# Kernel tuning notes

Hardware: AMD Instinct MI355X
Metric: run time of the kernel (lower is better)

The kernel has to match this reference:

```python
import jax, jax.numpy as jnp
import numpy as np

MAX_DEPTH = 9
HIDDEN = 64
EMB = 64
POS_FREQS = 6
IN_C = 1
SIZES = [4 ** d for d in range(MAX_DEPTH + 1)]
OFFSETS = np.concatenate([[0], np.cumsum(SIZES)])  # per-depth slices into concatenated node arrays
TOTAL = int(OFFSETS[-1])  # 349525
POS_DIM = 3 + 2 * POS_FREQS * 3  # 39


def _interleave(v):
    v = v & 0xFFFF
    v = (v | (v << 8)) & 0x00FF00FF
    v = (v | (v << 4)) & 0x0F0F0F0F
    v = (v | (v << 2)) & 0x33333333
    v = (v | (v << 1)) & 0x55555555
    return v


def _deinterleave(v):
    v = v & 0x55555555
    v = (v | (v >> 1)) & 0x33333333
    v = (v | (v >> 2)) & 0x0F0F0F0F
    v = (v | (v >> 4)) & 0x00FF00FF
    v = (v | (v >> 8)) & 0x0000FFFF
    return v


def _xy(d):
    keys = jnp.arange(4 ** d, dtype=jnp.int32)  # full tree: sorted Morton keys = arange
    return _deinterleave(keys), _deinterleave(keys >> 1)


def _neighbors(d):
    # [N, 9] neighbor indices in Morton order grid; -1 outside the image (matches quadtree.neighs padding)
    ix, iy = _xy(d)
    res = 1 << d
    cols = []
    for dy in (-1, 0, 1):
        for dx in (-1, 0, 1):
            nx, ny = ix + dx, iy + dy
            valid = (nx >= 0) & (nx < res) & (ny >= 0) & (ny < res)
            key = _interleave(nx) | (_interleave(ny) << 1)
            cols.append(jnp.where(valid, key, -1))
    return jnp.stack(cols, axis=1)


def _pos_enc(d):
    # node_centers_from_keys + fourier_encode
    ix, iy = _xy(d)
    res = float(1 << d)
    x = (ix.astype(jnp.float32) + 0.5) / res
    y = (iy.astype(jnp.float32) + 0.5) / res
    dn = jnp.full_like(x, float(d) / float(MAX_DEPTH))
    pos = jnp.stack([x, y, dn], axis=1)  # [N, 3]
    freqs = 2.0 ** jnp.arange(POS_FREQS, dtype=jnp.float32)
    ang = pos[:, :, None] * (2.0 * np.pi) * freqs  # [N, 3, F]
    enc = jnp.concatenate([jnp.sin(ang), jnp.cos(ang)], axis=-1).reshape(pos.shape[0], -1)  # [N, 3*2F]
    return jnp.concatenate([pos, enc], axis=1)  # [N, 39]


def setup_inputs() -> dict:
    key = jax.random.key(0)
    ks = jax.random.split(key, 10)
    s = 0.05
    return {
        "features_in": jax.random.normal(ks[0], (TOTAL, IN_C), jnp.float32),
        "in_proj_W": jax.random.normal(ks[1], (IN_C + POS_DIM, HIDDEN), jnp.float32) * s,
        "in_proj_b": jnp.zeros((HIDDEN,), jnp.float32),
        "conv_W": jax.random.normal(ks[2], (MAX_DEPTH + 1, 9 * HIDDEN, HIDDEN), jnp.float32) * s,
        "conv_b": jnp.zeros((MAX_DEPTH + 1, HIDDEN), jnp.float32),
        "emb_W": jax.random.normal(ks[3], (MAX_DEPTH + 1, HIDDEN, EMB), jnp.float32) * s,
        "emb_b": jnp.zeros((MAX_DEPTH + 1, EMB), jnp.float32),
        "ln_g": jnp.ones((MAX_DEPTH + 1, EMB), jnp.float32),
        "ln_b": jnp.zeros((MAX_DEPTH + 1, EMB), jnp.float32),
        "depth_gain": jnp.ones((MAX_DEPTH + 1,), jnp.float32),
    }


def reference(features_in, in_proj_W, in_proj_b, conv_W, conv_b, emb_W, emb_b, ln_g, ln_b, depth_gain):
    D = MAX_DEPTH
    # per-depth input projection with fourier positional encoding
    h = []
    for d in range(D + 1):
        f = features_in[OFFSETS[d]:OFFSETS[d + 1]]
        x = jnp.concatenate([f, _pos_enc(d)], axis=1)  # [N_d, in_c + 39]
        h.append(x @ in_proj_W + in_proj_b)
    # bottom-up: QuadPool (mean over 4 children; full tree => children of parent i are 4i..4i+3) + QuadConv
    for d in range(D, 0, -1):
        Np = 4 ** (d - 1)
        pooled = h[d].reshape(Np, 4, HIDDEN).mean(axis=1)
        hd1 = h[d - 1] + pooled
        if d - 1 >= 1:
            neigh = _neighbors(d - 1)  # [N, 9], -1 at borders
            N = neigh.shape[0]
            padded = jnp.concatenate([hd1, jnp.zeros((1, HIDDEN), hd1.dtype)], axis=0)
            gi = jnp.where(neigh < 0, N, neigh)
            col = padded[gi].reshape(N, 9 * HIDDEN)
            hd1 = jax.nn.relu(col @ conv_W[d - 1] + conv_b[d - 1])
        h[d - 1] = hd1
    # per-depth embedding head: Linear -> LayerNorm -> depth gain
    outs = []
    eps = 1e-5
    for d in range(D + 1):
        z = h[d] @ emb_W[d] + emb_b[d]
        mu = z.mean(-1, keepdims=True)
        var = ((z - mu) ** 2).mean(-1, keepdims=True)
        z = (z - mu) / jnp.sqrt(var + eps) * ln_g[d] + ln_b[d]
        outs.append(depth_gain[d] * z)
    return jnp.concatenate(outs, axis=0)  # [TOTAL, EMB] (E[0]..E[max_depth] concatenated)
```

## Files before the change

### kernel.cpp

```cpp
#include <hip/hip_runtime.h>
#include <hip/hip_bf16.h>

static constexpr int TOTAL = 349525;
static constexpr int OFFS[11] = {0,1,5,21,85,341,1365,5461,21845,87381,349525};
static constexpr int EB64[11] = {0,1,2,3,4,8,24,88,344,1368,5464};
static constexpr size_t CONV_USH = (size_t)8*9*2*4*64*8;
static constexpr size_t EMB_USH  = (size_t)10*2*4*64*8;
static constexpr size_t FRAG_USH = CONV_USH + EMB_USH;
static constexpr size_t FRAG_BYTES = FRAG_USH*2*2;
static constexpr size_t HPRE_BYTES = (size_t)(87381-85)*64*4;

typedef __attribute__((ext_vector_type(8))) short short8;
typedef __attribute__((ext_vector_type(4))) float f32x4;

__device__ __forceinline__ unsigned deint(unsigned v){
  v &= 0x55555555u;
  v = (v | (v>>1)) & 0x33333333u;
  v = (v | (v>>2)) & 0x0F0F0F0Fu;
  v = (v | (v>>4)) & 0x00FF00FFu;
  v = (v | (v>>8)) & 0x0000FFFFu;
  return v;
}
__device__ __forceinline__ unsigned ileave(unsigned v){
  v &= 0xFFFFu;
  v = (v | (v<<8)) & 0x00FF00FFu;
  v = (v | (v<<4)) & 0x0F0F0F0Fu;
  v = (v | (v<<2)) & 0x33333333u;
  v = (v | (v<<1)) & 0x55555555u;
  return v;
}
__device__ __forceinline__ unsigned short f2bh(float x){
  unsigned u = __float_as_uint(x);
  return (unsigned short)((u + 0x7FFFu + ((u>>16)&1u)) >> 16);
}
__device__ __forceinline__ float bh2f(unsigned short h){
  return __uint_as_float(((unsigned)h) << 16);
}
__device__ __forceinline__ void split8(float4 a, float4 b, short8 &hi, short8 &lo){
  float v[8] = {a.x,a.y,a.z,a.w,b.x,b.y,b.z,b.w};
  unsigned short hv[8], lv[8];
  #pragma unroll
  for (int j=0;j<8;++j){ hv[j]=f2bh(v[j]); lv[j]=f2bh(v[j]-bh2f(hv[j])); }
  hi = short8{(short)hv[0],(short)hv[1],(short)hv[2],(short)hv[3],
              (short)hv[4],(short)hv[5],(short)hv[6],(short)hv[7]};
  lo = short8{(short)lv[0],(short)lv[1],(short)lv[2],(short)lv[3],
              (short)lv[4],(short)lv[5],(short)lv[6],(short)lv[7]};
}

__global__ __launch_bounds__(256) void k_wprep(const float* __restrict__ convW,
    const float* __restrict__ embW,
    unsigned short* __restrict__ WH, unsigned short* __restrict__ WLo){
  int tid = blockIdx.x*256 + threadIdx.x;
  if (tid >= 41984) return;
  const float* src;
  size_t dst;
  if (tid < 36864){
    int l=tid&63, cb=(tid>>6)&3, ks=(tid>>8)&1;
    int x=tid>>9; int m=x%9, Lp=x/9;
    int k0=ks*32+((l>>4)<<3), ch=cb*16+(l&15);
    src = convW + (size_t)(Lp+1)*36864 + (size_t)(m*64+k0)*64 + ch;
    dst = (size_t)tid*8;
  } else {
    int t2 = tid - 36864;
    int l=t2&63, cb=(t2>>6)&3, ks=(t2>>8)&1, d=t2>>9;
    int k0=ks*32+((l>>4)<<3), ch=cb*16+(l&15);
    src = embW + (size_t)d*4096 + (size_t)k0*64 + ch;
    dst = CONV_USH + (size_t)t2*8;
  }
  unsigned short hv[8], lv[8];
  #pragma unroll
  for (int j=0;j<8;++j){
    float v = src[(size_t)j*64];
    unsigned short h = f2bh(v);
    hv[j] = h;
    lv[j] = f2bh(v - bh2f(h));
  }
  short8 vh = {(short)hv[0],(short)hv[1],(short)hv[2],(short)hv[3],
               (short)hv[4],(short)hv[5],(short)hv[6],(short)hv[7]};
  short8 vl = {(short)lv[0],(short)lv[1],(short)lv[2],(short)lv[3],
               (short)lv[4],(short)lv[5],(short)lv[6],(short)lv[7]};
  *(short8*)(WH  + dst) = vh;
  *(short8*)(WLo + dst) = vl;
}

__global__ __launch_bounds__(256) void k_inproj(const float* __restrict__ feat,
    const float* __restrict__ W, const float* __restrict__ B,
    float* __restrict__ h, float* __restrict__ hpre){
  __shared__ float Alt[128][44];
  __shared__ float Wl[40][68];
  int t = threadIdx.x;
  int base = blockIdx.x * 128;
  for (int idx = t; idx < 40*64; idx += 256)
    Wl[idx >> 6][idx & 63] = W[idx];
  if (t < 128){
    int g = base + t;
    float* row = Alt[t];
    if (g < TOTAL){
      int d = 0;
      #pragma unroll
      for (int i = 1; i <= 9; ++i) if (g >= OFFS[i]) d = i;
      int local = g - OFFS[d];
      unsigned ix = deint((unsigned)local), iy = deint(((unsigned)local) >> 1);
      float inv = 1.0f / (float)(1 << d);
      float px = ((float)ix + 0.5f) * inv;
      float py = ((float)iy + 0.5f) * inv;
      float pd = (float)d * (1.0f/9.0f);
      row[0] = feat[g]; row[1] = px; row[2] = py; row[3] = pd;
      float p3[3] = {px, py, pd};
      #pragma unroll
      for (int c = 0; c < 3; ++c){
        float s, co;
        __sincosf(6.28318530717958647692f * p3[c], &s, &co);
        float* rb = row + 4 + c*12;
        #pragma unroll
        for (int f = 0; f < 6; ++f){
          rb[f] = s; rb[6+f] = co;
          float s2 = 2.f*s*co, c2 = 1.f - 2.f*s*s;
          s = s2; co = c2;
        }
      }
    } else {
      #pragma unroll
      for (int k = 0; k < 40; ++k) row[k] = 0.f;
    }
  }
  __syncthreads();
  int tr = t >> 3, tc = t & 7;
  float acc[4][8];
  #pragma unroll
  for (int i=0;i<4;++i)
    #pragma unroll
    for (int c=0;c<8;++c) acc[i][c] = 0.f;
  #pragma unroll 2
  for (int k4 = 0; k4 < 10; ++k4){
    float av4[4][4];
    #pragma unroll
    for (int i=0;i<4;++i){
      float4 aa = *(const float4*)&Alt[tr*4+i][k4*4];
      av4[i][0]=aa.x; av4[i][1]=aa.y; av4[i][2]=aa.z; av4[i][3]=aa.w;
    }
    #pragma unroll
    for (int j=0;j<4;++j){
      float4 lo = *(const float4*)&Wl[k4*4+j][tc*8];
      float4 hi = *(const float4*)&Wl[k4*4+j][tc*8+4];
      float wv[8];
      wv[0]=lo.x; wv[1]=lo.y; wv[2]=lo.z; wv[3]=lo.w;
      wv[4]=hi.x; wv[5]=hi.y; wv[6]=hi.z; wv[7]=hi.w;
      #pragma unroll
      for (int i=0;i<4;++i){
        float a = av4[i][j];
        #pragma unroll
        for (int c=0;c<8;++c) acc[i][c] += a*wv[c];
      }
    }
  }
  #pragma unroll
  for (int i=0;i<4;++i){
    int g = base + tr*4 + i;
    if (g >= TOTAL) continue;
    float ov[8];
    #pragma unroll
    for (int c=0;c<8;++c) ov[c] = acc[i][c] + B[tc*8+c];
    float* dst = &h[(size_t)g*64 + tc*8];
    *(float4*)dst       = *(const float4*)&ov[0];
    *(float4*)(dst + 4) = *(const float4*)&ov[4];
    if (hpre && g >= OFFS[4] && g < OFFS[9]){
      float* dp = hpre + (size_t)(g - OFFS[4])*64 + tc*8;
      *(float4*)dp       = *(const float4*)&ov[0];
      *(float4*)(dp + 4) = *(const float4*)&ov[4];
    }
  }
}

__global__ __launch_bounds__(256) void k_conv(float* __restrict__ h,
    const float* __restrict__ hPar,
    const unsigned short* __restrict__ WHl, const unsigned short* __restrict__ WLl,
    const float* __restrict__ Bb, int N, int offL, int offC, int lbits){
  __shared__ unsigned short haloH[100*72];
  __shared__ unsigned short haloL[100*72];
  __shared__ int hkey[100];
  int t = threadIdx.x;
  int nb = blockIdx.x * 64;
  int res = 1 << lbits;
  if (t < 100){
    int i = t % 10, j = t / 10;
    int gx = (int)deint((unsigned)nb) - 1 + i;
    int gy = (int)deint(((unsigned)nb)>>1) - 1 + j;
    bool ok = (gx>=0 && gy>=0 && gx<res && gy<res);
    hkey[t] = ok ? (int)(ileave((unsigned)gx) | (ileave((unsigned)gy)<<1)) : -1;
  }
  __syncthreads();
  const float* hC = h + (size_t)offC*64;
  for (int e = t; e < 1600; e += 256){
    int hi_ = e >> 4, u = e & 15;
    int key = hkey[hi_];
    float4 r = make_float4(0.f,0.f,0.f,0.f);
    if (key >= 0){
      const float4* c = (const float4*)(hC + (size_t)(4*key)*64) + u;
      float4 c0 = c[0], c1 = c[16], c2 = c[32], c3 = c[48];
      float4 pr = *((const float4*)(hPar + (size_t)key*64) + u);
      r.x = 0.25f*(c0.x+c1.x+c2.x+c3.x) + pr.x;
      r.y = 0.25f*(c0.y+c1.y+c2.y+c3.y) + pr.y;
      r.z = 0.25f*(c0.z+c1.z+c2.z+c3.z) + pr.z;
      r.w = 0.25f*(c0.w+c1.w+c2.w+c3.w) + pr.w;
    }
    unsigned short h0=f2bh(r.x), h1=f2bh(r.y), h2=f2bh(r.z), h3=f2bh(r.w);
    ushort4 rh = make_ushort4(h0,h1,h2,h3);
    ushort4 rl = make_ushort4(f2bh(r.x - bh2f(h0)), f2bh(r.y - bh2f(h1)),
                              f2bh(r.z - bh2f(h2)), f2bh(r.w - bh2f(h3)));
    *(ushort4*)&haloH[hi_*72 + u*4] = rh;
    *(ushort4*)&haloL[hi_*72 + u*4] = rl;
  }
  __syncthreads();

  int cb   = __builtin_amdgcn_readfirstlane((int)(threadIdx.x >> 6));
  int lane = t & 63;
  int q = lane >> 4;
  int chl = cb*16 + (lane & 15);
  int lx0,ly0,lx1,ly1,lx2,ly2,lx3,ly3;
  {
    int n0 = (lane&15), n1 = 16+(lane&15), n2 = 32+(lane&15), n3 = 48+(lane&15);
    lx0=(int)deint((unsigned)n0); ly0=(int)deint(((unsigned)n0)>>1);
    lx1=(int)deint((unsigned)n1); ly1=(int)deint(((unsigned)n1)>>1);
    lx2=(int)deint((unsigned)n2); ly2=(int)deint(((unsigned)n2)>>1);
    lx3=(int)deint((unsigned)n3); ly3=(int)deint(((unsigned)n3)>>1);
  }
  f32x4 acc0 = {0.f,0.f,0.f,0.f}, acc1 = acc0, acc2 = acc0, acc3 = acc0;

  #pragma unroll 1
  for (int dy=0;dy<3;++dy){
    #pragma unroll 1
    for (int dx=0;dx<3;++dx){
      int m = dy*3 + dx;
      int r0 = (ly0+dy)*10 + lx0+dx;
      int r1 = (ly1+dy)*10 + lx1+dx;
      int r2 = (ly2+dy)*10 + lx2+dx;
      int r3 = (ly3+dy)*10 + lx3+dx;
      #pragma unroll
      for (int ks=0;ks<2;++ks){
        const unsigned short* fp = WHl + ((size_t)((m*2+ks)*4 + cb)*64 + lane)*8;
        const unsigned short* fq = WLl + ((size_t)((m*2+ks)*4 + cb)*64 + lane)*8;
        short8 bh = *(const short8*)fp;
        short8 bl = *(const short8*)fq;
        int so = (ks*4 + q)*8;
        short8 ah0 = *(const short8*)&haloH[r0*72 + so];
        short8 al0 = *(const short8*)&haloL[r0*72 + so];
        short8 ah1 = *(const short8*)&haloH[r1*72 + so];
        short8 al1 = *(const short8*)&haloL[r1*72 + so];
        short8 ah2 = *(const short8*)&haloH[r2*72 + so];
        short8 al2 = *(const short8*)&haloL[r2*72 + so];
        short8 ah3 = *(const short8*)&haloH[r3*72 + so];
        short8 al3 = *(const short8*)&haloL[r3*72 + so];
        acc0 = __builtin_amdgcn_mfma_f32_16x16x32_bf16(ah0, bh, acc0, 0,0,0);
        acc1 = __builtin_amdgcn_mfma_f32_16x16x32_bf16(ah1, bh, acc1, 0,0,0);
        acc2 = __builtin_amdgcn_mfma_f32_16x16x32_bf16(ah2, bh, acc2, 0,0,0);
        acc3 = __builtin_amdgcn_mfma_f32_16x16x32_bf16(ah3, bh, acc3, 0,0,0);
        acc0 = __builtin_amdgcn_mfma_f32_16x16x32_bf16(al0, bh, acc0, 0,0,0);
        acc1 = __builtin_amdgcn_mfma_f32_16x16x32_bf16(al1, bh, acc1, 0,0,0);
        acc2 = __builtin_amdgcn_mfma_f32_16x16x32_bf16(al2, bh, acc2, 0,0,0);
        acc3 = __builtin_amdgcn_mfma_f32_16x16x32_bf16(al3, bh, acc3, 0,0,0);
        acc0 = __builtin_amdgcn_mfma_f32_16x16x32_bf16(ah0, bl, acc0, 0,0,0);
        acc1 = __builtin_amdgcn_mfma_f32_16x16x32_bf16(ah1, bl, acc1, 0,0,0);
        acc2 = __builtin_amdgcn_mfma_f32_16x16x32_bf16(ah2, bl, acc2, 0,0,0);
        acc3 = __builtin_amdgcn_mfma_f32_16x16x32_bf16(ah3, bl, acc3, 0,0,0);
      }
    }
  }
  float bias = Bb[chl];
  int rowb = q*4;
  float* hO = h + (size_t)(offL + nb)*64;
  #pragma unroll
  for (int reg=0;reg<4;++reg){
    int n0 = rowb + reg;
    float v0 = acc0[reg] + bias; if (nb + n0      < N) hO[(size_t)(n0     )*64 + chl] = v0 > 0.f ? v0 : 0.f;
    float v1 = acc1[reg] + bias; if (nb + n0 + 16 < N) hO[(size_t)(n0 + 16)*64 + chl] = v1 > 0.f ? v1 : 0.f;
    float v2 = acc2[reg] + bias; if (nb + n0 + 32 < N) hO[(size_t)(n0 + 32)*64 + chl] = v2 > 0.f ? v2 : 0.f;
    float v3 = acc3[reg] + bias; if (nb + n0 + 48 < N) hO[(size_t)(n0 + 48)*64 + chl] = v3 > 0.f ? v3 : 0.f;
  }
}

template<int L>
__device__ __forceinline__ void tail_level2(float* __restrict__ h,
    const unsigned short* __restrict__ WHc, const unsigned short* __restrict__ WLc,
    const float* __restrict__ convB, const float* __restrict__ Hpar,
    unsigned short* __restrict__ PtH, unsigned short* __restrict__ PtL, int t){
  constexpr int Np  = 1 << (2*L);
  constexpr int NTt = (Np + 15)/16;
  constexpr int TG  = (NTt + 3)/4;
  constexpr int res = 1 << L;
  int w  = t >> 6;
  int cb = __builtin_amdgcn_readfirstlane(w & 3);
  int tg = __builtin_amdgcn_readfirstlane(w >> 2);
  int lane = t & 63;
  int q = lane >> 4, li = lane & 15;
  int chl = cb*16 + li;
  int lx[TG], ly[TG];
  #pragma unroll
  for (int i=0;i<TG;++i){
    unsigned n = (unsigned)((tg*TG + i)*16 + li);
    lx[i] = (int)deint(n); ly[i] = (int)deint(n >> 1);
  }
  f32x4 acc[TG];
  #pragma unroll
  for (int i=0;i<TG;++i) acc[i] = f32x4{0.f,0.f,0.f,0.f};
  short8 bh0, bl0, bh1, bl1;
  {
    size_t f0 = ((size_t)(0*4 + cb)*64 + lane)*8;
    size_t f1 = ((size_t)(1*4 + cb)*64 + lane)*8;
    bh0 = *(const short8*)(WHc + f0); bl0 = *(const short8*)(WLc + f0);
    bh1 = *(const short8*)(WHc + f1); bl1 = *(const short8*)(WLc + f1);
  }
  #pragma unroll 1
  for (int m=0;m<9;++m){
    short8 nh0, nl0, nh1, nl1;
    if (m < 8){
      size_t f0 = ((size_t)(((m+1)*2+0)*4 + cb)*64 + lane)*8;
      size_t f1 = ((size_t)(((m+1)*2+1)*4 + cb)*64 + lane)*8;
      nh0 = *(const short8*)(WHc + f0); nl0 = *(const short8*)(WLc + f0);
      nh1 = *(const short8*)(WHc + f1); nl1 = *(const short8*)(WLc + f1);
    }
    int dy = m/3 - 1, dx = m%3 - 1;
    #pragma unroll
    for (int i=0;i<TG;++i){
      int nx = lx[i]+dx, ny = ly[i]+dy;
      int key = (nx>=0 && ny>=0 && nx<res && ny<res)
              ? (int)(ileave((unsigned)nx) | (ileave((unsigned)ny)<<1)) : Np;
      const unsigned short* pH = PtH + key*72;
      const unsigned short* pL = PtL + key*72;
      short8 ah0 = *(const short8*)(pH + q*8);
      short8 al0 = *(const short8*)(pL + q*8);
      short8 ah1 = *(const short8*)(pH + 32 + q*8);
      short8 al1 = *(const short8*)(pL + 32 + q*8);
      acc[i] = __builtin_amdgcn_mfma_f32_16x16x32_bf16(ah0, bh0, acc[i], 0,0,0);
      acc[i] = __builtin_amdgcn_mfma_f32_16x16x32_bf16(al0, bh0, acc[i], 0,0,0);
      acc[i] = __builtin_amdgcn_mfma_f32_16x16x32_bf16(ah0, bl0, acc[i], 0,0,0);
      acc[i] = __builtin_amdgcn_mfma_f32_16x16x32_bf16(ah1, bh1, acc[i], 0,0,0);
      acc[i] = __builtin_amdgcn_mfma_f32_16x16x32_bf16(al1, bh1, acc[i], 0,0,0);
      acc[i] = __builtin_amdgcn_mfma_f32_16x16x32_bf16(ah1, bl1, acc[i], 0,0,0);
    }
    if (m < 8){ bh0 = nh0; bl0 = nl0; bh1 = nh1; bl1 = nl1; }
  }
  float bias = convB[L*64 + chl];
  float vq[TG][4];
  #pragma unroll
  for (int i=0;i<TG;++i){
    #pragma unroll
    for (int reg=0;reg<4;++reg){
      int ni = (tg*TG + i)*16 + q*4 + reg;
      float v = acc[i][reg] + bias;
      v = v > 0.f ? v : 0.f;
      vq[i][reg] = v;
      if (ni < Np) h[(size_t)(OFFS[L] + ni)*64 + chl] = v;
    }
  }
  __syncthreads();
  if (L > 1){
    constexpr int Pp = Np/4;
    #pragma unroll
    for (int i=0;i<TG;++i){
      int p = (tg*TG + i)*4 + q;
      if (p < Pp){
        float pooled = 0.25f*(vq[i][0]+vq[i][1]+vq[i][2]+vq[i][3])
                     + Hpar[(size_t)(OFFS[L-1] + p)*64 + chl];
        unsigned short hh = f2bh(pooled);
        PtH[p*72 + chl] = hh;
        PtL[p*72 + chl] = f2bh(pooled - bh2f(hh));
      }
    }
    if (t < 64){ PtH[Pp*72 + t] = 0; PtL[Pp*72 + t] = 0; }
  } else {
    if (tg == 0 && q == 0){
      float pooled = 0.25f*(vq[0][0]+vq[0][1]+vq[0][2]+vq[0][3]) + Hpar[chl];
      h[chl] = pooled;
    }
  }
  __syncthreads();
}

__global__ __launch_bounds__(1024) void k_tail(float* __restrict__ h,
    const unsigned short* __restrict__ WH, const unsigned short* __restrict__ WLo,
    const float* __restrict__ convB){
  __shared__ unsigned short PtH[257*72];
  __shared__ unsigned short PtL[257*72];
  __shared__ float Hpar[85*64];
  int t = threadIdx.x;
  for (int e = t; e < 85*16; e += 1024)
    ((float4*)Hpar)[e] = ((const float4*)h)[e];
  for (int e = t; e < 257*16; e += 1024){
    int node = e >> 4, u = e & 15;
    float4 r = make_float4(0.f,0.f,0.f,0.f);
    if (node < 256){
      const float4* c = (const float4*)(h + (size_t)(OFFS[5] + 4*node)*64) + u;
      float4 c0 = c[0], c1 = c[16], c2 = c[32], c3 = c[48];
      float4 pr = *((const float4*)(h + (size_t)(OFFS[4] + node)*64) + u);
      r.x = 0.25f*(c0.x+c1.x+c2.x+c3.x) + pr.x;
      r.y = 0.25f*(c0.y+c1.y+c2.y+c3.y) + pr.y;
      r.z = 0.25f*(c0.z+c1.z+c2.z+c3.z) + pr.z;
      r.w = 0.25f*(c0.w+c1.w+c2.w+c3.w) + pr.w;
    }
    unsigned short h0=f2bh(r.x), h1=f2bh(r.y), h2=f2bh(r.z), h3=f2bh(r.w);
    *(ushort4*)&PtH[node*72 + u*4] = make_ushort4(h0,h1,h2,h3);
    *(ushort4*)&PtL[node*72 + u*4] = make_ushort4(
        f2bh(r.x - bh2f(h0)), f2bh(r.y - bh2f(h1)),
        f2bh(r.z - bh2f(h2)), f2bh(r.w - bh2f(h3)));
  }
  __syncthreads();
  tail_level2<4>(h, WH + (size_t)3*36864, WLo + (size_t)3*36864, convB, Hpar, PtH, PtL, t);
  tail_level2<3>(h, WH + (size_t)2*36864, WLo + (size_t)2*36864, convB, Hpar, PtH, PtL, t);
  tail_level2<2>(h, WH + (size_t)1*36864, WLo + (size_t)1*36864, convB, Hpar, PtH, PtL, t);
  tail_level2<1>(h, WH,                   WLo,                   convB, Hpar, PtH, PtL, t);
}

__global__ __launch_bounds__(256) void k_emb(float* __restrict__ h,
    const unsigned short* __restrict__ EH, const unsigned short* __restrict__ ELo,
    const float* __restrict__ embB, const float* __restrict__ lng,
    const float* __restrict__ lnb, const float* __restrict__ gain){
  int bb = blockIdx.x;
  int d = 0;
  #pragma unroll
  for (int i=1;i<=9;++i) if (bb >= EB64[i]) d = i;
  int nb = (bb - EB64[d]) * 64;
  int N = 1 << (2*d);
  int off = OFFS[d];
  int t = threadIdx.x;
  int wt = __builtin_amdgcn_readfirstlane(t >> 6);
  int lane = t & 63;
  int q = lane >> 4, li = lane & 15;

  const float* rp = h + ((size_t)off + nb + wt*16 + li)*64 + q*8;
  float4 a0 = *(const float4*)rp;
  float4 a1 = *(const float4*)(rp + 4);
  float4 a2 = *(const float4*)(rp + 32);
  float4 a3 = *(const float4*)(rp + 36);
  short8 ah0, al0, ah1, al1;
  split8(a0, a1, ah0, al0);
  split8(a2, a3, ah1, al1);

  f32x4 acc0 = {0.f,0.f,0.f,0.f}, acc1 = acc0, acc2 = acc0, acc3 = acc0;
  #define EMB_CB(CB, ACC) { \
    size_t f0 = (((size_t)(d*2+0)*4 + (CB))*64 + lane)*8; \
    size_t f1 = (((size_t)(d*2+1)*4 + (CB))*64 + lane)*8; \
    short8 bh0 = *(const short8*)(EH + f0); \
    short8 bl0 = *(const short8*)(ELo + f0); \
    short8 bh1 = *(const short8*)(EH + f1); \
    short8 bl1 = *(const short8*)(ELo + f1); \
    ACC = __builtin_amdgcn_mfma_f32_16x16x32_bf16(ah0, bh0, ACC, 0,0,0); \
    ACC = __builtin_amdgcn_mfma_f32_16x16x32_bf16(al0, bh0, ACC, 0,0,0); \
    ACC = __builtin_amdgcn_mfma_f32_16x16x32_bf16(ah0, bl0, ACC, 0,0,0); \
    ACC = __builtin_amdgcn_mfma_f32_16x16x32_bf16(ah1, bh1, ACC, 0,0,0); \
    ACC = __builtin_amdgcn_mfma_f32_16x16x32_bf16(al1, bh1, ACC, 0,0,0); \
    ACC = __builtin_amdgcn_mfma_f32_16x16x32_bf16(ah1, bl1, ACC, 0,0,0); }
  EMB_CB(0, acc0)
  EMB_CB(1, acc1)
  EMB_CB(2, acc2)
  EMB_CB(3, acc3)
  #undef EMB_CB

  float b0 = embB[d*64 +      li];
  float b1 = embB[d*64 + 16 + li];
  float b2 = embB[d*64 + 32 + li];
  float b3 = embB[d*64 + 48 + li];
  float mu[4], rs[4];
  float z0[4], z1[4], z2[4], z3[4];
  #pragma unroll
  for (int r=0;r<4;++r){
    z0[r] = acc0[r] + b0;
    z1[r] = acc1[r] + b1;
    z2[r] = acc2[r] + b2;
    z3[r] = acc3[r] + b3;
    float s  = z0[r] + z1[r] + z2[r] + z3[r];
    float qv = z0[r]*z0[r] + z1[r]*z1[r] + z2[r]*z2[r] + z3[r]*z3[r];
    #pragma unroll
    for (int mk=1; mk<16; mk<<=1){
      s  += __shfl_xor(s, mk, 64);
      qv += __shfl_xor(qv, mk, 64);
    }
    float m = s * 0.015625f;
    mu[r] = m;
    rs[r] = rsqrtf(qv * 0.015625f - m*m + 1e-5f);
  }
  float g0 = lng[d*64 +      li], l0 = lnb[d*64 +      li];
  float g1 = lng[d*64 + 16 + li], l1 = lnb[d*64 + 16 + li];
  float g2 = lng[d*64 + 32 + li], l2 = lnb[d*64 + 32 + li];
  float g3 = lng[d*64 + 48 + li], l3 = lnb[d*64 + 48 + li];
  float gn = gain[d];
  #pragma unroll
  for (int r=0;r<4;++r){
    int ni = wt*16 + q*4 + r;
    if (nb + ni < N){
      float* row = h + ((size_t)off + nb + ni)*64;
      row[     li] = ((z0[r] - mu[r])*rs[r]*g0 + l0)*gn;
      row[16 + li] = ((z1[r] - mu[r])*rs[r]*g1 + l1)*gn;
      row[32 + li] = ((z2[r] - mu[r])*rs[r]*g2 + l2)*gn;
      row[48 + li] = ((z3[r] - mu[r])*rs[r]*g3 + l3)*gn;
    }
  }
}

extern "C" void kernel_launch(void* const* d_in, const int* in_sizes, int n_in,
                              void* d_out, int out_size, void* d_ws, size_t ws_size,
                              hipStream_t stream) {
  (void)in_sizes; (void)n_in; (void)out_size;
  const float* feat  = (const float*)d_in[0];
  const float* ipW   = (const float*)d_in[1];
  const float* ipB   = (const float*)d_in[2];
  const float* convW = (const float*)d_in[3];
  const float* convB = (const float*)d_in[4];
  const float* embW  = (const float*)d_in[5];
  const float* embB  = (const float*)d_in[6];
  const float* lng   = (const float*)d_in[7];
  const float* lnb   = (const float*)d_in[8];
  const float* gain  = (const float*)d_in[9];
  float* h = (float*)d_out;

  unsigned short* WH  = (unsigned short*)d_ws;
  unsigned short* WLo = WH + FRAG_USH;
  float* hpre = (ws_size >= FRAG_BYTES + HPRE_BYTES)
              ? (float*)((char*)d_ws + FRAG_BYTES) : nullptr;

  k_wprep<<<164, 256, 0, stream>>>(convW, embW, WH, WLo);
  k_inproj<<<(TOTAL + 127)/128, 256, 0, stream>>>(feat, ipW, ipB, h, hpre);

  for (int L = 8; L >= 5; --L){
    int Np = 1 << (2*L);
    const float* hPar = hpre ? (hpre + (size_t)(OFFS[L] - OFFS[4])*64)
                             : (h + (size_t)OFFS[L]*64);
    k_conv<<<Np/64, 256, 0, stream>>>(h, hPar,
        WH  + (size_t)(L-1)*36864, WLo + (size_t)(L-1)*36864,
        convB + (size_t)L*64, Np, OFFS[L], OFFS[L+1], L);
  }

  k_tail<<<1, 1024, 0, stream>>>(h, WH, WLo, convB);
  k_emb<<<5464, 256, 0, stream>>>(h, WH + CONV_USH, WLo + CONV_USH,
                                  embB, lng, lnb, gain);
}
```

Baseline: 205.6 us.

## Fuse tail conv levels with embedding head into one launch

```diff
diff --git a/kernel.cpp b/kernel.cpp
--- a/kernel.cpp
+++ b/kernel.cpp
@@ -3,7 +3,6 @@
 
 static constexpr int TOTAL = 349525;
 static constexpr int OFFS[11] = {0,1,5,21,85,341,1365,5461,21845,87381,349525};
-static constexpr int EB64[11] = {0,1,2,3,4,8,24,88,344,1368,5464};
 static constexpr size_t CONV_USH = (size_t)8*9*2*4*64*8;
 static constexpr size_t EMB_USH  = (size_t)10*2*4*64*8;
 static constexpr size_t FRAG_USH = CONV_USH + EMB_USH;
@@ -279,155 +278,13 @@
   }
 }
 
-template<int L>
-__device__ __forceinline__ void tail_level2(float* __restrict__ h,
-    const unsigned short* __restrict__ WHc, const unsigned short* __restrict__ WLc,
-    const float* __restrict__ convB, const float* __restrict__ Hpar,
-    unsigned short* __restrict__ PtH, unsigned short* __restrict__ PtL, int t){
-  constexpr int Np  = 1 << (2*L);
-  constexpr int NTt = (Np + 15)/16;
-  constexpr int TG  = (NTt + 3)/4;
-  constexpr int res = 1 << L;
-  int w  = t >> 6;
-  int cb = __builtin_amdgcn_readfirstlane(w & 3);
-  int tg = __builtin_amdgcn_readfirstlane(w >> 2);
-  int lane = t & 63;
-  int q = lane >> 4, li = lane & 15;
-  int chl = cb*16 + li;
-  int lx[TG], ly[TG];
-  #pragma unroll
-  for (int i=0;i<TG;++i){
-    unsigned n = (unsigned)((tg*TG + i)*16 + li);
-    lx[i] = (int)deint(n); ly[i] = (int)deint(n >> 1);
-  }
-  f32x4 acc[TG];
-  #pragma unroll
-  for (int i=0;i<TG;++i) acc[i] = f32x4{0.f,0.f,0.f,0.f};
-  short8 bh0, bl0, bh1, bl1;
-  {
-    size_t f0 = ((size_t)(0*4 + cb)*64 + lane)*8;
-    size_t f1 = ((size_t)(1*4 + cb)*64 + lane)*8;
-    bh0 = *(const short8*)(WHc + f0); bl0 = *(const short8*)(WLc + f0);
-    bh1 = *(const short8*)(WHc + f1); bl1 = *(const short8*)(WLc + f1);
-  }
-  #pragma unroll 1
-  for (int m=0;m<9;++m){
-    short8 nh0, nl0, nh1, nl1;
-    if (m < 8){
-      size_t f0 = ((size_t)(((m+1)*2+0)*4 + cb)*64 + lane)*8;
-      size_t f1 = ((size_t)(((m+1)*2+1)*4 + cb)*64 + lane)*8;
-      nh0 = *(const short8*)(WHc + f0); nl0 = *(const short8*)(WLc + f0);
-      nh1 = *(const short8*)(WHc + f1); nl1 = *(const short8*)(WLc + f1);
-    }
-    int dy = m/3 - 1, dx = m%3 - 1;
-    #pragma unroll
-    for (int i=0;i<TG;++i){
-      int nx = lx[i]+dx, ny = ly[i]+dy;
-      int key = (nx>=0 && ny>=0 && nx<res && ny<res)
-              ? (int)(ileave((unsigned)nx) | (ileave((unsigned)ny)<<1)) : Np;
-      const unsigned short* pH = PtH + key*72;
-      const unsigned short* pL = PtL + key*72;
-      short8 ah0 = *(const short8*)(pH + q*8);
-      short8 al0 = *(const short8*)(pL + q*8);
-      short8 ah1 = *(const short8*)(pH + 32 + q*8);
-      short8 al1 = *(const short8*)(pL + 32 + q*8);
-      acc[i] = __builtin_amdgcn_mfma_f32_16x16x32_bf16(ah0, bh0, acc[i], 0,0,0);
-      acc[i] = __builtin_amdgcn_mfma_f32_16x16x32_bf16(al0, bh0, acc[i], 0,0,0);
-      acc[i] = __builtin_amdgcn_mfma_f32_16x16x32_bf16(ah0, bl0, acc[i], 0,0,0);
-      acc[i] = __builtin_amdgcn_mfma_f32_16x16x32_bf16(ah1, bh1, acc[i], 0,0,0);
-      acc[i] = __builtin_amdgcn_mfma_f32_16x16x32_bf16(al1, bh1, acc[i], 0,0,0);
-      acc[i] = __builtin_amdgcn_mfma_f32_16x16x32_bf16(ah1, bl1, acc[i], 0,0,0);
-    }
-    if (m < 8){ bh0 = nh0; bl0 = nl0; bh1 = nh1; bl1 = nl1; }
-  }
-  float bias = convB[L*64 + chl];
-  float vq[TG][4];
-  #pragma unroll
-  for (int i=0;i<TG;++i){
-    #pragma unroll
-    for (int reg=0;reg<4;++reg){
-      int ni = (tg*TG + i)*16 + q*4 + reg;
-      float v = acc[i][reg] + bias;
-      v = v > 0.f ? v : 0.f;
-      vq[i][reg] = v;
-      if (ni < Np) h[(size_t)(OFFS[L] + ni)*64 + chl] = v;
-    }
-  }
-  __syncthreads();
-  if (L > 1){
-    constexpr int Pp = Np/4;
-    #pragma unroll
-    for (int i=0;i<TG;++i){
-      int p = (tg*TG + i)*4 + q;
-      if (p < Pp){
-        float pooled = 0.25f*(vq[i][0]+vq[i][1]+vq[i][2]+vq[i][3])
-                     + Hpar[(size_t)(OFFS[L-1] + p)*64 + chl];
-        unsigned short hh = f2bh(pooled);
-        PtH[p*72 + chl] = hh;
-        PtL[p*72 + chl] = f2bh(pooled - bh2f(hh));
-      }
-    }
-    if (t < 64){ PtH[Pp*72 + t] = 0; PtL[Pp*72 + t] = 0; }
-  } else {
-    if (tg == 0 && q == 0){
-      float pooled = 0.25f*(vq[0][0]+vq[0][1]+vq[0][2]+vq[0][3]) + Hpar[chl];
-      h[chl] = pooled;
-    }
-  }
-  __syncthreads();
-}
-
-__global__ __launch_bounds__(1024) void k_tail(float* __restrict__ h,
-    const unsigned short* __restrict__ WH, const unsigned short* __restrict__ WLo,
-    const float* __restrict__ convB){
-  __shared__ unsigned short PtH[257*72];
-  __shared__ unsigned short PtL[257*72];
-  __shared__ float Hpar[85*64];
-  int t = threadIdx.x;
-  for (int e = t; e < 85*16; e += 1024)
-    ((float4*)Hpar)[e] = ((const float4*)h)[e];
-  for (int e = t; e < 257*16; e += 1024){
-    int node = e >> 4, u = e & 15;
-    float4 r = make_float4(0.f,0.f,0.f,0.f);
-    if (node < 256){
-      const float4* c = (const float4*)(h + (size_t)(OFFS[5] + 4*node)*64) + u;
-      float4 c0 = c[0], c1 = c[16], c2 = c[32], c3 = c[48];
-      float4 pr = *((const float4*)(h + (size_t)(OFFS[4] + node)*64) + u);
-      r.x = 0.25f*(c0.x+c1.x+c2.x+c3.x) + pr.x;
-      r.y = 0.25f*(c0.y+c1.y+c2.y+c3.y) + pr.y;
-      r.z = 0.25f*(c0.z+c1.z+c2.z+c3.z) + pr.z;
-      r.w = 0.25f*(c0.w+c1.w+c2.w+c3.w) + pr.w;
-    }
-    unsigned short h0=f2bh(r.x), h1=f2bh(r.y), h2=f2bh(r.z), h3=f2bh(r.w);
-    *(ushort4*)&PtH[node*72 + u*4] = make_ushort4(h0,h1,h2,h3);
-    *(ushort4*)&PtL[node*72 + u*4] = make_ushort4(
-        f2bh(r.x - bh2f(h0)), f2bh(r.y - bh2f(h1)),
-        f2bh(r.z - bh2f(h2)), f2bh(r.w - bh2f(h3)));
-  }
-  __syncthreads();
-  tail_level2<4>(h, WH + (size_t)3*36864, WLo + (size_t)3*36864, convB, Hpar, PtH, PtL, t);
-  tail_level2<3>(h, WH + (size_t)2*36864, WLo + (size_t)2*36864, convB, Hpar, PtH, PtL, t);
-  tail_level2<2>(h, WH + (size_t)1*36864, WLo + (size_t)1*36864, convB, Hpar, PtH, PtL, t);
-  tail_level2<1>(h, WH,                   WLo,                   convB, Hpar, PtH, PtL, t);
-}
-
-__global__ __launch_bounds__(256) void k_emb(float* __restrict__ h,
+__device__ __forceinline__ void emb_tile(float* __restrict__ h,
     const unsigned short* __restrict__ EH, const unsigned short* __restrict__ ELo,
     const float* __restrict__ embB, const float* __restrict__ lng,
-    const float* __restrict__ lnb, const float* __restrict__ gain){
-  int bb = blockIdx.x;
-  int d = 0;
-  #pragma unroll
-  for (int i=1;i<=9;++i) if (bb >= EB64[i]) d = i;
-  int nb = (bb - EB64[d]) * 64;
-  int N = 1 << (2*d);
-  int off = OFFS[d];
-  int t = threadIdx.x;
-  int wt = __builtin_amdgcn_readfirstlane(t >> 6);
-  int lane = t & 63;
+    const float* __restrict__ lnb, const float* __restrict__ gain,
+    int d, size_t rowbase, int validN, int lane){
   int q = lane >> 4, li = lane & 15;
-
-  const float* rp = h + ((size_t)off + nb + wt*16 + li)*64 + q*8;
+  const float* rp = h + (rowbase + li)*64 + q*8;
   float4 a0 = *(const float4*)rp;
   float4 a1 = *(const float4*)(rp + 4);
   float4 a2 = *(const float4*)(rp + 32);
@@ -435,7 +292,6 @@
   short8 ah0, al0, ah1, al1;
   split8(a0, a1, ah0, al0);
   split8(a2, a3, ah1, al1);
-
   f32x4 acc0 = {0.f,0.f,0.f,0.f}, acc1 = acc0, acc2 = acc0, acc3 = acc0;
   #define EMB_CB(CB, ACC) { \
     size_t f0 = (((size_t)(d*2+0)*4 + (CB))*64 + lane)*8; \
@@ -455,7 +311,6 @@
   EMB_CB(2, acc2)
   EMB_CB(3, acc3)
   #undef EMB_CB
-
   float b0 = embB[d*64 +      li];
   float b1 = embB[d*64 + 16 + li];
   float b2 = embB[d*64 + 32 + li];
@@ -486,14 +341,175 @@
   float gn = gain[d];
   #pragma unroll
   for (int r=0;r<4;++r){
-    int ni = wt*16 + q*4 + r;
-    if (nb + ni < N){
-      float* row = h + ((size_t)off + nb + ni)*64;
+    int ni = q*4 + r;
+    if (ni < validN){
+      float* row = h + (rowbase + ni)*64;
       row[     li] = ((z0[r] - mu[r])*rs[r]*g0 + l0)*gn;
       row[16 + li] = ((z1[r] - mu[r])*rs[r]*g1 + l1)*gn;
       row[32 + li] = ((z2[r] - mu[r])*rs[r]*g2 + l2)*gn;
       row[48 + li] = ((z3[r] - mu[r])*rs[r]*g3 + l3)*gn;
     }
+  }
+}
+
+template<int L>
+__device__ __forceinline__ void tail_level2(float* __restrict__ h,
+    const unsigned short* __restrict__ WHc, const unsigned short* __restrict__ WLc,
+    const float* __restrict__ convB, const float* __restrict__ Hpar,
+    unsigned short* __restrict__ PtH, unsigned short* __restrict__ PtL, int t){
+  constexpr int Np  = 1 << (2*L);
+  constexpr int NTt = (Np + 15)/16;
+  constexpr int TG  = (NTt + 3)/4;
+  constexpr int res = 1 << L;
+  int w  = t >> 6;
+  int cb = __builtin_amdgcn_readfirstlane(w & 3);
+  int tg = __builtin_amdgcn_readfirstlane(w >> 2);
+  int lane = t & 63;
+  int q = lane >> 4, li = lane & 15;
+  int chl = cb*16 + li;
+  int lx[TG], ly[TG];
+  #pragma unroll
+  for (int i=0;i<TG;++i){
+    unsigned n = (unsigned)((tg*TG + i)*16 + li);
+    lx[i] = (int)deint(n); ly[i] = (int)deint(n >> 1);
+  }
+  f32x4 acc[TG];
+  #pragma unroll
+  for (int i=0;i<TG;++i) acc[i] = f32x4{0.f,0.f,0.f,0.f};
+  short8 bh0, bl0, bh1, bl1;
+  {
+    size_t f0 = ((size_t)(0*4 + cb)*64 + lane)*8;
+    size_t f1 = ((size_t)(1*4 + cb)*64 + lane)*8;
+    bh0 = *(const short8*)(WHc + f0); bl0 = *(const short8*)(WLc + f0);
+    bh1 = *(const short8*)(WHc + f1); bl1 = *(const short8*)(WLc + f1);
+  }
+  #pragma unroll 1
+  for (int m=0;m<9;++m){
+    short8 nh0, nl0, nh1, nl1;
+    if (m < 8){
+      size_t f0 = ((size_t)(((m+1)*2+0)*4 + cb)*64 + lane)*8;
+      size_t f1 = ((size_t)(((m+1)*2+1)*4 + cb)*64 + lane)*8;
+      nh0 = *(const short8*)(WHc + f0); nl0 = *(const short8*)(WLc + f0);
+      nh1 = *(const short8*)(WHc + f1); nl1 = *(const short8*)(WLc + f1);
+    }
+    int dy = m/3 - 1, dx = m%3 - 1;
+    #pragma unroll
+    for (int i=0;i<TG;++i){
+      int nx = lx[i]+dx, ny = ly[i]+dy;
+      int key = (nx>=0 && ny>=0 && nx<res && ny<res)
+              ? (int)(ileave((unsigned)nx) | (ileave((unsigned)ny)<<1)) : Np;
+      const unsigned short* pH = PtH + key*72;
+      const unsigned short* pL = PtL + key*72;
+      short8 ah0 = *(const short8*)(pH + q*8);
+      short8 al0 = *(const short8*)(pL + q*8);
+      short8 ah1 = *(const short8*)(pH + 32 + q*8);
+      short8 al1 = *(const short8*)(pL + 32 + q*8);
+      acc[i] = __builtin_amdgcn_mfma_f32_16x16x32_bf16(ah0, bh0, acc[i], 0,0,0);
+      acc[i] = __builtin_amdgcn_mfma_f32_16x16x32_bf16(al0, bh0, acc[i], 0,0,0);
+      acc[i] = __builtin_amdgcn_mfma_f32_16x16x32_bf16(ah0, bl0, acc[i], 0,0,0);
+      acc[i] = __builtin_amdgcn_mfma_f32_16x16x32_bf16(ah1, bh1, acc[i], 0,0,0);
+      acc[i] = __builtin_amdgcn_mfma_f32_16x16x32_bf16(al1, bh1, acc[i], 0,0,0);
+      acc[i] = __builtin_amdgcn_mfma_f32_16x16x32_bf16(ah1, bl1, acc[i], 0,0,0);
+    }
+    if (m < 8){ bh0 = nh0; bl0 = nl0; bh1 = nh1; bl1 = nl1; }
+  }
+  float bias = convB[L*64 + chl];
+  float vq[TG][4];
+  #pragma unroll
+  for (int i=0;i<TG;++i){
+    #pragma unroll
+    for (int reg=0;reg<4;++reg){
+      int ni = (tg*TG + i)*16 + q*4 + reg;
+      float v = acc[i][reg] + bias;
+      v = v > 0.f ? v : 0.f;
+      vq[i][reg] = v;
+      if (ni < Np) h[(size_t)(OFFS[L] + ni)*64 + chl] = v;
+    }
+  }
+  __syncthreads();
+  if (L > 1){
+    constexpr int Pp = Np/4;
+    #pragma unroll
+    for (int i=0;i<TG;++i){
+      int p = (tg*TG + i)*4 + q;
+      if (p < Pp){
+        float pooled = 0.25f*(vq[i][0]+vq[i][1]+vq[i][2]+vq[i][3])
+                     + Hpar[(size_t)(OFFS[L-1] + p)*64 + chl];
+        unsigned short hh = f2bh(pooled);
+        PtH[p*72 + chl] = hh;
+        PtL[p*72 + chl] = f2bh(pooled - bh2f(hh));
+      }
+    }
+    if (t < 64){ PtH[Pp*72 + t] = 0; PtL[Pp*72 + t] = 0; }
+  } else {
+    if (tg == 0 && q == 0){
+      float pooled = 0.25f*(vq[0][0]+vq[0][1]+vq[0][2]+vq[0][3]) + Hpar[chl];
+      h[chl] = pooled;
+    }
+  }
+  __syncthreads();
+}
+
+__global__ __launch_bounds__(1024) void k_tail_emb(float* __restrict__ h,
+    const unsigned short* __restrict__ WH, const unsigned short* __restrict__ WLo,
+    const float* __restrict__ convB,
+    const unsigned short* __restrict__ EH, const unsigned short* __restrict__ ELo,
+    const float* __restrict__ embB, const float* __restrict__ lng,
+    const float* __restrict__ lnb, const float* __restrict__ gain){
+  __shared__ unsigned short PtH[257*72];
+  __shared__ unsigned short PtL[257*72];
+  __shared__ float Hpar[85*64];
+  int t = threadIdx.x;
+  if (blockIdx.x != 0){
+    int bb = blockIdx.x - 1;
+    int d, start;
+    if      (bb < 8)  { d=6; start=0;   }
+    else if (bb < 40) { d=7; start=8;   }
+    else if (bb < 168){ d=8; start=40;  }
+    else              { d=9; start=168; }
+    size_t base = (size_t)OFFS[d] + (size_t)(bb - start)*512;
+    int w = t >> 6, lane = t & 63;
+    emb_tile(h, EH, ELo, embB, lng, lnb, gain, d, base + (size_t)w*16,      16, lane);
+    emb_tile(h, EH, ELo, embB, lng, lnb, gain, d, base + (size_t)(w+16)*16, 16, lane);
+    return;
+  }
+  for (int e = t; e < 85*16; e += 1024)
+    ((float4*)Hpar)[e] = ((const float4*)h)[e];
+  for (int e = t; e < 257*16; e += 1024){
+    int node = e >> 4, u = e & 15;
+    float4 r = make_float4(0.f,0.f,0.f,0.f);
+    if (node < 256){
+      const float4* c = (const float4*)(h + (size_t)(OFFS[5] + 4*node)*64) + u;
+      float4 c0 = c[0], c1 = c[16], c2 = c[32], c3 = c[48];
+      float4 pr = *((const float4*)(h + (size_t)(OFFS[4] + node)*64) + u);
+      r.x = 0.25f*(c0.x+c1.x+c2.x+c3.x) + pr.x;
+      r.y = 0.25f*(c0.y+c1.y+c2.y+c3.y) + pr.y;
+      r.z = 0.25f*(c0.z+c1.z+c2.z+c3.z) + pr.z;
+      r.w = 0.25f*(c0.w+c1.w+c2.w+c3.w) + pr.w;
+    }
+    unsigned short h0=f2bh(r.x), h1=f2bh(r.y), h2=f2bh(r.z), h3=f2bh(r.w);
+    *(ushort4*)&PtH[node*72 + u*4] = make_ushort4(h0,h1,h2,h3);
+    *(ushort4*)&PtL[node*72 + u*4] = make_ushort4(
+        f2bh(r.x - bh2f(h0)), f2bh(r.y - bh2f(h1)),
+        f2bh(r.z - bh2f(h2)), f2bh(r.w - bh2f(h3)));
+  }
+  __syncthreads();
+  tail_level2<4>(h, WH + (size_t)3*36864, WLo + (size_t)3*36864, convB, Hpar, PtH, PtL, t);
+  tail_level2<3>(h, WH + (size_t)2*36864, WLo + (size_t)2*36864, convB, Hpar, PtH, PtL, t);
+  tail_level2<2>(h, WH + (size_t)1*36864, WLo + (size_t)1*36864, convB, Hpar, PtH, PtL, t);
+  tail_level2<1>(h, WH,                   WLo,                   convB, Hpar, PtH, PtL, t);
+  int w = t >> 6, lane = t & 63;
+  for (int j = w; j < 87; j += 16){
+    int d, tile;
+    if (j < 64)      { d=5; tile=j;    }
+    else if (j < 80) { d=4; tile=j-64; }
+    else if (j < 84) { d=3; tile=j-80; }
+    else if (j == 84){ d=2; tile=0;    }
+    else if (j == 85){ d=1; tile=0;    }
+    else             { d=0; tile=0;    }
+    int Nlev = 1 << (2*d);
+    emb_tile(h, EH, ELo, embB, lng, lnb, gain, d,
+             (size_t)OFFS[d] + (size_t)tile*16, Nlev - tile*16, lane);
   }
 }
 
@@ -530,7 +546,6 @@
         convB + (size_t)L*64, Np, OFFS[L], OFFS[L+1], L);
   }
 
-  k_tail<<<1, 1024, 0, stream>>>(h, WH, WLo, convB);
-  k_emb<<<5464, 256, 0, stream>>>(h, WH + CONV_USH, WLo + CONV_USH,
-                                  embB, lng, lnb, gain);
-}
+  k_tail_emb<<<681, 1024, 0, stream>>>(h, WH, WLo, convB,
+      WH + CONV_USH, WLo + CONV_USH, embB, lng, lnb, gain);
+}
```

Measured after the change: 205.8 us. About the same (+0.1%).
